# Performance work log

Hardware: AMD Instinct MI355X
Metric: run time of the kernel (lower is better)

Reference implementation:

```python
import jax, jax.numpy as jnp
import numpy as np

N_NODES = 100000
N_EDGES = 1600000
N_HOPS = 3
D_FEAT = 128
D_HID = 256
NUM_GRAPHS = 64


def setup_inputs() -> dict:
    key = jax.random.key(0)
    ks = jax.random.split(key, 8)
    x = jax.random.normal(ks[0], (N_NODES, D_FEAT), dtype=jnp.float32)
    edge_index = jax.random.randint(ks[1], (N_HOPS, 2, N_EDGES), 0, N_NODES, dtype=jnp.int64)
    edge_weight = jax.random.uniform(ks[2], (N_HOPS, N_EDGES), dtype=jnp.float32)
    batch = jnp.sort(jax.random.randint(ks[3], (N_NODES,), 0, NUM_GRAPHS, dtype=jnp.int64))
    w1 = jax.random.normal(ks[4], (D_FEAT, D_HID), dtype=jnp.float32) * (1.0 / np.sqrt(D_FEAT))
    b1 = jnp.zeros((D_HID,), dtype=jnp.float32)
    w2 = jax.random.normal(ks[5], (D_HID, D_FEAT), dtype=jnp.float32) * (1.0 / np.sqrt(D_HID))
    b2 = jnp.zeros((D_FEAT,), dtype=jnp.float32)
    prop_w = jnp.ones((N_HOPS + 1,), dtype=jnp.float32)
    return {"x": x, "edge_index": edge_index, "edge_weight": edge_weight,
            "batch": batch, "w1": w1, "b1": b1, "w2": w2, "b2": b2, "prop_w": prop_w}


def reference(x, edge_index, edge_weight, batch, w1, b1, w2, b2, prop_w):
    n = x.shape[0]
    # MLP: dropout is identity in eval mode
    h = jax.nn.relu(x @ w1 + b1)          # [N, hid]
    h = h @ w2 + b2                        # [N, feat]
    # prop_weight: weighted sum over hops; hop i uses edge_index[layers[i]-1]
    acc = prop_w[0] * h
    for i in range(edge_index.shape[0]):
        src = edge_index[i, 0]             # x_j source nodes
        dst = edge_index[i, 1]             # aggregation targets
        msg = edge_weight[i][:, None] * h[src]              # [E, feat]
        agg = jax.ops.segment_sum(msg, dst, num_segments=n)  # [N, feat]
        acc = acc + prop_w[i + 1] * agg
    # sum over hop dim already folded into acc; global_add_pool over graphs
    pooled = jax.ops.segment_sum(acc, batch, num_segments=NUM_GRAPHS)  # [G, feat]
    # original returns log_softmax of pooled features (lin3 output is unused)
    return jax.nn.log_softmax(pooled, axis=1)
```

## Files before the change

kernel.cpp:

```cpp
#include <hip/hip_runtime.h>
#include <hip/hip_bf16.h>


#define N_NODES 100000
#define N_EDGES 1600000
#define N_HOPS 3
#define D_HID 256
#define N_GRAPHS 64

#define CHUNK 32
#define NCHUNK 3125
#define FG 512

#define NB 625
#define RB 160
#define SGRID 500
#define SB 1024
#define I4PB 2400
#define NI4H 400000
#define STAGE_W 11475
#define RSTRIDE 11840

#define CT_OFF    0u
#define BU8_OFF   0u
#define REC_OFF   12800000u
#define SPART_OFF REC_OFF
#define OFFS_OFF  36500000u
#define SMALL_OFF 40000000u
#define TGR_OFF   SMALL_OFF
#define SSUM_OFF  (SMALL_OFF + 32768u)
#define W1P_OFF   (SMALL_OFF + 131072u)

typedef __attribute__((ext_vector_type(4))) float f32x4;
typedef __attribute__((ext_vector_type(8))) short s16x8;
typedef __attribute__((ext_vector_type(4))) int i32x4;
typedef __attribute__((ext_vector_type(4))) float fv4;

__device__ __forceinline__ unsigned short f2bf_rne(float f) {
    union { float f; unsigned u; } v; v.f = f;
    unsigned r = v.u + 0x7FFFu + ((v.u >> 16) & 1u);
    return (unsigned short)(r >> 16);
}
__device__ __forceinline__ float bf2f(unsigned short s) {
    union { float f; unsigned u; } v; v.u = ((unsigned)s) << 16;
    return v.f;
}
__device__ __forceinline__ unsigned pk_rne(float lo, float hi) {
    return ((unsigned)f2bf_rne(hi) << 16) | (unsigned)f2bf_rne(lo);
}

__global__ __launch_bounds__(256) void prep_kernel(const float* __restrict__ w1,
                                                   unsigned short* __restrict__ w1p,
                                                   const int* __restrict__ batch,
                                                   unsigned char* __restrict__ bu8) {
    if (blockIdx.x < 16) {
        int f = blockIdx.x * 256 + threadIdx.x;
        int t = f >> 4, fr = f & 15, nt = fr >> 2, ks = fr & 3;
        int w = t >> 6, l = t & 63, q = l >> 4, c = l & 15;
        s16x8 v;
#pragma unroll
        for (int j = 0; j < 8; j++)
            v[j] = (short)f2bf_rne(w1[(size_t)(32 * ks + 8 * q + j) * 256 + w * 64 + 16 * nt + c]);
        *(s16x8*)&w1p[(size_t)f * 8] = v;
    } else {
        int i = (blockIdx.x - 16) * 1024 + threadIdx.x * 4;
        if (i < N_NODES) {
            int4 v = *(const int4*)&batch[i];
            uchar4 o;
            o.x = (unsigned char)v.x; o.y = (unsigned char)v.y;
            o.z = (unsigned char)v.z; o.w = (unsigned char)v.w;
            *(uchar4*)&bu8[i] = o;
        }
    }
}

__global__ __launch_bounds__(SB) void scatter_kernel(
    const int* __restrict__ ei, const float* __restrict__ ew,
    const unsigned char* __restrict__ bu8, const float* __restrict__ pw,
    unsigned* __restrict__ offs, unsigned* __restrict__ records) {
    __shared__ unsigned cnt[NB], lbase[NB], ccnt[NB];
    __shared__ unsigned wtot[16];
    __shared__ unsigned tot;
    __shared__ unsigned stage[STAGE_W];
    const int tid = threadIdx.x;
    const int lane = tid & 63, wid = tid >> 6;
    const int i40 = blockIdx.x * I4PB;

    if (tid < NB) cnt[tid] = 0u;
    __syncthreads();

    const float pw1 = pw[1], pw2 = pw[2], pw3 = pw[3];

    unsigned rec[12], bkt[12];
#pragma unroll
    for (int k = 0; k < 3; k++) {
        int idx = tid + k * SB;
        if (idx < I4PB) {
            int i4 = i40 + idx;
            unsigned hop = (unsigned)i4 / NI4H;
            int r4 = i4 - (int)hop * NI4H;
            const i32x4* sp4 = (const i32x4*)(ei + (size_t)hop * 2 * N_EDGES);
            i32x4 s = __builtin_nontemporal_load(sp4 + r4);
            i32x4 d = __builtin_nontemporal_load(sp4 + NI4H + r4);
            fv4 wv = __builtin_nontemporal_load((const fv4*)(ew + (size_t)hop * N_EDGES) + r4);
            float pwh = hop == 0 ? pw1 : (hop == 1 ? pw2 : pw3);
#pragma unroll
            for (int j = 0; j < 4; j++) {
                unsigned b = (unsigned)s[j] / RB;
                bkt[k * 4 + j] = b;
                rec[k * 4 + j] = ((unsigned)f2bf_rne(pwh * wv[j]) << 16) |
                                 (unsigned)(((unsigned)s[j] - b * RB) * 64 + (unsigned)bu8[d[j]]);
                atomicAdd(&cnt[b], 1u);
            }
        } else {
#pragma unroll
            for (int j = 0; j < 4; j++) bkt[k * 4 + j] = 0xFFFFFFFFu;
        }
    }
    __syncthreads();

    unsigned pcv = 0;
    if (tid < NB) {
        unsigned cc = cnt[tid];
        ccnt[tid] = cc;
        pcv = (cc + 3u) & ~3u;
        cnt[tid] = 0u;
    }
    unsigned inc = pcv;
#pragma unroll
    for (int d = 1; d < 64; d <<= 1) {
        unsigned u = __shfl_up(inc, d, 64);
        if (lane >= d) inc += u;
    }
    if (lane == 63) wtot[wid] = inc;
    __syncthreads();
    if (tid < 16) {
        unsigned wv = wtot[tid];
        unsigned winc = wv;
#pragma unroll
        for (int d = 1; d < 16; d <<= 1) {
            unsigned u = __shfl_up(winc, d, 16);
            if ((tid & 15) >= d) winc += u;
        }
        wtot[tid] = winc - wv;
    }
    __syncthreads();
    if (tid < NB) {
        unsigned lb = inc - pcv + wtot[wid];
        lbase[tid] = lb;
        offs[(size_t)blockIdx.x * NB + tid] = (pcv << 16) | lb;
        if (tid == NB - 1) tot = lb + pcv;
        for (unsigned i = ccnt[tid]; i < pcv; i++) stage[lb + i] = 0u;
    }
    __syncthreads();

#pragma unroll
    for (int k = 0; k < 12; k++) {
        if (bkt[k] != 0xFFFFFFFFu) {
            unsigned o = atomicAdd(&cnt[bkt[k]], 1u);
            stage[lbase[bkt[k]] + o] = rec[k];
        }
    }
    __syncthreads();

    unsigned total = tot;
    unsigned* dst = records + (size_t)blockIdx.x * RSTRIDE;
    for (unsigned i = tid * 4; i < total; i += SB * 4) {
        *(uint4*)&dst[i] = *(const uint4*)&stage[i];
    }
}

__global__ __launch_bounds__(512) void phaseB_kernel(
    const int* __restrict__ batch, const float* __restrict__ pw,
    const unsigned* __restrict__ offs, const unsigned* __restrict__ records,
    unsigned short* __restrict__ ct, float* __restrict__ tgr) {
    __shared__ float tile[RB * 64];
    const int tid = threadIdx.x;
    const int b = blockIdx.x;
    const int grp = tid >> 3, gl = tid & 7;

    for (int i = tid; i < RB * 64; i += 512) tile[i] = 0.f;
    __syncthreads();

    if (tid < RB) atomicAdd(&tile[tid * 64 + batch[b * RB + tid]], pw[0]);

    for (int t = grp; t < SGRID; t += 64) {
        unsigned w = offs[(size_t)t * NB + b];
        const unsigned* rp = records + (size_t)t * RSTRIDE + (w & 0xFFFFu);
        unsigned pc = w >> 16;
        for (unsigned base = 4u * gl; base < pc; base += 32u) {
            uint4 r4 = *(const uint4*)(rp + base);
            unsigned m0 = r4.x & 0x3FFFu, m1 = r4.y & 0x3FFFu;
            unsigned m2 = r4.z & 0x3FFFu, m3 = r4.w & 0x3FFFu;
            atomicAdd(&tile[m0], bf2f((unsigned short)(r4.x >> 16)));
            atomicAdd(&tile[m1], bf2f((unsigned short)(r4.y >> 16)));
            atomicAdd(&tile[m2], bf2f((unsigned short)(r4.z >> 16)));
            atomicAdd(&tile[m3], bf2f((unsigned short)(r4.w >> 16)));
        }
    }
    __syncthreads();

    if (tid < 256) {
        const int gt = tid >> 6, l = tid & 63, q = l >> 4, c = l & 15;
        for (int cc = 0; cc < 5; cc++) {
            s16x8 v;
#pragma unroll
            for (int j = 0; j < 8; j++)
                v[j] = (short)f2bf_rne(tile[(cc * 32 + 8 * q + j) * 64 + 16 * gt + c]);
            *(s16x8*)&ct[(((size_t)(b * 5 + cc) * 4 + gt) * 64 + l) * 8] = v;
        }
    }
    if (tid < 64) {
        float sum = 0.f;
        for (int s = 0; s < RB; s++) sum += tile[s * 64 + tid];
        atomicAdd(&tgr[(b & 63) * 64 + tid], sum);
    }
}

__global__ __launch_bounds__(256, 2) void fused_kernel(
    const float* __restrict__ x,
    const unsigned short* __restrict__ w1p,
    const float* __restrict__ b1,
    const unsigned short* __restrict__ ct,
    unsigned short* __restrict__ s_part) {

    __shared__ __align__(16) unsigned short Ut[256 * 40];
    __shared__ __align__(16) unsigned short x_lds[32 * 136];
    __shared__ __align__(16) unsigned short ct_lds[2048];

    const int tid = threadIdx.x;
    const int w = tid >> 6, l = tid & 63, q = l >> 4, c = l & 15;
    const int wcol = w * 64;
    const int sr = tid >> 3, sk = (tid & 7) * 16;

    s16x8 w1f[4][4];
    {
        const s16x8* wp = (const s16x8*)(w1p + (size_t)tid * 128);
#pragma unroll
        for (int nt = 0; nt < 4; nt++)
#pragma unroll
            for (int ks = 0; ks < 4; ks++)
                w1f[nt][ks] = wp[nt * 4 + ks];
    }

    float bias[4];
#pragma unroll
    for (int nt = 0; nt < 4; nt++) bias[nt] = b1[wcol + 16 * nt + c];

    f32x4 sacc[4][4];
#pragma unroll
    for (int gt = 0; gt < 4; gt++)
#pragma unroll
        for (int nt = 0; nt < 4; nt++) sacc[gt][nt] = (f32x4)0.f;

    uint4 xp0, xp1;
    s16x8 ctp;

#define PREF(CI)                                                              \
    {                                                                         \
        const float4* p = (const float4*)&x[(size_t)((CI) * 32 + sr) * 128 + sk]; \
        float4 v0 = p[0], v1 = p[1], v2 = p[2], v3 = p[3];                    \
        xp0.x = pk_rne(v0.x, v0.y); xp0.y = pk_rne(v0.z, v0.w);               \
        xp0.z = pk_rne(v1.x, v1.y); xp0.w = pk_rne(v1.z, v1.w);               \
        xp1.x = pk_rne(v2.x, v2.y); xp1.y = pk_rne(v2.z, v2.w);               \
        xp1.z = pk_rne(v3.x, v3.y); xp1.w = pk_rne(v3.z, v3.w);               \
        ctp = *(const s16x8*)&ct[(size_t)(CI) * 2048 + tid * 8];              \
    }

    int ci = blockIdx.x;
    if (ci < NCHUNK) PREF(ci);

    for (; ci < NCHUNK; ci += FG) {
        *(uint4*)&x_lds[sr * 136 + sk] = xp0;
        *(uint4*)&x_lds[sr * 136 + sk + 8] = xp1;
        *(s16x8*)&ct_lds[tid * 8] = ctp;
        __syncthreads();

        s16x8 af[2][4], ctf[4];
#pragma unroll
        for (int mt = 0; mt < 2; mt++)
#pragma unroll
            for (int ks = 0; ks < 4; ks++)
                af[mt][ks] = *(const s16x8*)&x_lds[(16 * mt + c) * 136 + 32 * ks + 8 * q];
#pragma unroll
        for (int gt = 0; gt < 4; gt++)
            ctf[gt] = *(const s16x8*)&ct_lds[(gt * 64 + l) * 8];
        __syncthreads();

        if (ci + FG < NCHUNK) PREF(ci + FG);

        f32x4 u[2][4];
#pragma unroll
        for (int mt = 0; mt < 2; mt++)
#pragma unroll
            for (int nt = 0; nt < 4; nt++) {
                f32x4 a; a[0] = a[1] = a[2] = a[3] = bias[nt];
                u[mt][nt] = a;
            }
#pragma unroll
        for (int ks = 0; ks < 4; ks++)
#pragma unroll
            for (int mt = 0; mt < 2; mt++)
#pragma unroll
                for (int nt = 0; nt < 4; nt++)
                    u[mt][nt] = __builtin_amdgcn_mfma_f32_16x16x32_bf16(
                        af[mt][ks], w1f[nt][ks], u[mt][nt], 0, 0, 0);

#pragma unroll
        for (int mt = 0; mt < 2; mt++)
#pragma unroll
            for (int nt = 0; nt < 4; nt++) {
                f32x4 v = u[mt][nt];
                uint2 d;
                d.x = pk_rne(fmaxf(v[0], 0.f), fmaxf(v[1], 0.f));
                d.y = pk_rne(fmaxf(v[2], 0.f), fmaxf(v[3], 0.f));
                *(uint2*)&Ut[(wcol + 16 * nt + c) * 40 + 16 * mt + 4 * q] = d;
            }

#pragma unroll
        for (int nt = 0; nt < 4; nt++) {
            s16x8 uf = *(const s16x8*)&Ut[(wcol + 16 * nt + c) * 40 + 8 * q];
#pragma unroll
            for (int gt = 0; gt < 4; gt++)
                sacc[gt][nt] = __builtin_amdgcn_mfma_f32_16x16x32_bf16(
                    ctf[gt], uf, sacc[gt][nt], 0, 0, 0);
        }
    }
#undef PREF

    unsigned short* my = s_part + (size_t)blockIdx.x * (64 * 256);
#pragma unroll
    for (int gt = 0; gt < 4; gt++)
#pragma unroll
        for (int nt = 0; nt < 4; nt++)
#pragma unroll
            for (int r = 0; r < 4; r++)
                my[(16 * gt + 4 * q + r) * 256 + wcol + 16 * nt + c] =
                    f2bf_rne(sacc[gt][nt][r]);
}

__global__ __launch_bounds__(256) void reduce_kernel(const unsigned short* __restrict__ s_part,
                                                     float* __restrict__ s_sum) {
    __shared__ float red[4][64];
    const int l = threadIdx.x & 63, p = threadIdx.x >> 6;
    const int e = blockIdx.x * 64 + l;
    float a0 = 0.f, a1 = 0.f, a2 = 0.f, a3 = 0.f;
    for (int b = p * (FG / 4); b < (p + 1) * (FG / 4); b += 4) {
        a0 += bf2f(s_part[(size_t)(b + 0) * 16384 + e]);
        a1 += bf2f(s_part[(size_t)(b + 1) * 16384 + e]);
        a2 += bf2f(s_part[(size_t)(b + 2) * 16384 + e]);
        a3 += bf2f(s_part[(size_t)(b + 3) * 16384 + e]);
    }
    red[p][l] = (a0 + a1) + (a2 + a3);
    __syncthreads();
    if (p == 0) s_sum[e] = (red[0][l] + red[1][l]) + (red[2][l] + red[3][l]);
}

__global__ void finalize_kernel(const float* __restrict__ s,
                                const float* __restrict__ tgr,
                                const float* __restrict__ w2,
                                const float* __restrict__ b2,
                                float* __restrict__ out) {
    __shared__ float red[128];
    __shared__ float tgs;
    const int g = blockIdx.x;
    const int f = threadIdx.x;

    if (f < 64) {
        float v = tgr[f * 64 + g];
        for (int off = 32; off; off >>= 1) v += __shfl_down(v, off, 64);
        if (f == 0) tgs = v;
    }
    __syncthreads();

    float acc = tgs * b2[f];
    for (int k = 0; k < D_HID; k++)
        acc += s[(size_t)g * 256 + k] * w2[(size_t)k * 128 + f];

    red[f] = acc;
    __syncthreads();
    for (int off = 64; off > 0; off >>= 1) {
        if (f < off) red[f] = fmaxf(red[f], red[f + off]);
        __syncthreads();
    }
    float mx = red[0];
    __syncthreads();
    red[f] = expf(acc - mx);
    __syncthreads();
    for (int off = 64; off > 0; off >>= 1) {
        if (f < off) red[f] += red[f + off];
        __syncthreads();
    }
    float lse = logf(red[0]);
    out[(size_t)g * 128 + f] = acc - mx - lse;
}

extern "C" void kernel_launch(void* const* d_in, const int* in_sizes, int n_in,
                              void* d_out, int out_size, void* d_ws, size_t ws_size,
                              hipStream_t stream) {
    const float* x     = (const float*)d_in[0];
    const int*   ei    = (const int*)d_in[1];
    const float* ew    = (const float*)d_in[2];
    const int*   batch = (const int*)d_in[3];
    const float* w1    = (const float*)d_in[4];
    const float* b1    = (const float*)d_in[5];
    const float* w2    = (const float*)d_in[6];
    const float* b2    = (const float*)d_in[7];
    const float* pw    = (const float*)d_in[8];
    float* out = (float*)d_out;

    unsigned short* ctp     = (unsigned short*)((char*)d_ws + CT_OFF);
    unsigned char*  bu8     = (unsigned char*)((char*)d_ws + BU8_OFF);
    unsigned*       records = (unsigned*)((char*)d_ws + REC_OFF);
    unsigned short* s_part  = (unsigned short*)((char*)d_ws + SPART_OFF);
    unsigned*       offsp   = (unsigned*)((char*)d_ws + OFFS_OFF);
    float*          tgrp    = (float*)((char*)d_ws + TGR_OFF);
    float*          s_sum   = (float*)((char*)d_ws + SSUM_OFF);
    unsigned short* w1pp    = (unsigned short*)((char*)d_ws + W1P_OFF);

    hipMemsetAsync(tgrp, 0, 64 * 64 * sizeof(float), stream);

    prep_kernel<<<dim3(114), 256, 0, stream>>>(w1, w1pp, batch, bu8);
    scatter_kernel<<<dim3(SGRID), SB, 0, stream>>>(
        ei, ew, bu8, pw, offsp, records);
    phaseB_kernel<<<dim3(NB), 512, 0, stream>>>(batch, pw, offsp, records, ctp, tgrp);
    fused_kernel<<<dim3(FG), 256, 0, stream>>>(x, w1pp, b1, ctp, s_part);
    reduce_kernel<<<dim3(256), 256, 0, stream>>>(s_part, s_sum);
    finalize_kernel<<<dim3(64), 128, 0, stream>>>(s_sum, tgrp, w2, b2, out);
}
```

Measured before the change: 228.8 us.

## Replace two-pass bucketed scatter with direct global float atomics into coefficient matrix

The block-level bucket sort of edges into staged records, followed by a shared-memory accumulation pass, is replaced by a single kernel that does global float atomicAdd straight into a zeroed 100000x64 coefficient matrix C. A convert kernel then loads C tiles, adds the self term and emits the bf16 tiles. The aim is to drop the record write and read-back and the sorting overhead. In exchange it adds a 25.6MB memset and 4.8M scattered global atomics, which can contend. It also makes the accumulation order nondeterministic.

```diff
diff --git a/kernel.cpp b/kernel.cpp
--- a/kernel.cpp
+++ b/kernel.cpp
@@ -14,18 +14,15 @@
 
 #define NB 625
 #define RB 160
-#define SGRID 500
-#define SB 1024
-#define I4PB 2400
+#define NI4G 1200000
 #define NI4H 400000
-#define STAGE_W 11475
-#define RSTRIDE 11840
+#define AGG_BLOCKS 2048
+#define AGG_THREADS (AGG_BLOCKS * 256)
 
 #define CT_OFF    0u
-#define BU8_OFF   0u
-#define REC_OFF   12800000u
-#define SPART_OFF REC_OFF
-#define OFFS_OFF  36500000u
+#define C_OFF     12800000u
+#define SPART_OFF C_OFF
+#define BU8_OFF   38400000u
 #define SMALL_OFF 40000000u
 #define TGR_OFF   SMALL_OFF
 #define SSUM_OFF  (SMALL_OFF + 32768u)
@@ -74,130 +71,42 @@
     }
 }
 
-__global__ __launch_bounds__(SB) void scatter_kernel(
+__global__ __launch_bounds__(256) void agg_kernel(
     const int* __restrict__ ei, const float* __restrict__ ew,
     const unsigned char* __restrict__ bu8, const float* __restrict__ pw,
-    unsigned* __restrict__ offs, unsigned* __restrict__ records) {
-    __shared__ unsigned cnt[NB], lbase[NB], ccnt[NB];
-    __shared__ unsigned wtot[16];
-    __shared__ unsigned tot;
-    __shared__ unsigned stage[STAGE_W];
-    const int tid = threadIdx.x;
-    const int lane = tid & 63, wid = tid >> 6;
-    const int i40 = blockIdx.x * I4PB;
-
-    if (tid < NB) cnt[tid] = 0u;
-    __syncthreads();
-
+    float* __restrict__ C) {
     const float pw1 = pw[1], pw2 = pw[2], pw3 = pw[3];
-
-    unsigned rec[12], bkt[12];
-#pragma unroll
-    for (int k = 0; k < 3; k++) {
-        int idx = tid + k * SB;
-        if (idx < I4PB) {
-            int i4 = i40 + idx;
-            unsigned hop = (unsigned)i4 / NI4H;
-            int r4 = i4 - (int)hop * NI4H;
-            const i32x4* sp4 = (const i32x4*)(ei + (size_t)hop * 2 * N_EDGES);
-            i32x4 s = __builtin_nontemporal_load(sp4 + r4);
-            i32x4 d = __builtin_nontemporal_load(sp4 + NI4H + r4);
-            fv4 wv = __builtin_nontemporal_load((const fv4*)(ew + (size_t)hop * N_EDGES) + r4);
-            float pwh = hop == 0 ? pw1 : (hop == 1 ? pw2 : pw3);
-#pragma unroll
-            for (int j = 0; j < 4; j++) {
-                unsigned b = (unsigned)s[j] / RB;
-                bkt[k * 4 + j] = b;
-                rec[k * 4 + j] = ((unsigned)f2bf_rne(pwh * wv[j]) << 16) |
-                                 (unsigned)(((unsigned)s[j] - b * RB) * 64 + (unsigned)bu8[d[j]]);
-                atomicAdd(&cnt[b], 1u);
-            }
-        } else {
-#pragma unroll
-            for (int j = 0; j < 4; j++) bkt[k * 4 + j] = 0xFFFFFFFFu;
+    int gid = blockIdx.x * 256 + threadIdx.x;
+    for (int i4 = gid; i4 < NI4G; i4 += AGG_THREADS) {
+        unsigned hop = (unsigned)i4 / NI4H;
+        int r4 = i4 - (int)hop * NI4H;
+        const i32x4* sp4 = (const i32x4*)(ei + (size_t)hop * 2 * N_EDGES);
+        i32x4 s = __builtin_nontemporal_load(sp4 + r4);
+        i32x4 d = __builtin_nontemporal_load(sp4 + NI4H + r4);
+        fv4 wv = __builtin_nontemporal_load((const fv4*)(ew + (size_t)hop * N_EDGES) + r4);
+        float pwh = hop == 0 ? pw1 : (hop == 1 ? pw2 : pw3);
+#pragma unroll
+        for (int j = 0; j < 4; j++) {
+            unsigned g = bu8[d[j]];
+            atomicAdd(&C[(size_t)(unsigned)s[j] * 64 + g], pwh * wv[j]);
         }
     }
-    __syncthreads();
-
-    unsigned pcv = 0;
-    if (tid < NB) {
-        unsigned cc = cnt[tid];
-        ccnt[tid] = cc;
-        pcv = (cc + 3u) & ~3u;
-        cnt[tid] = 0u;
-    }
-    unsigned inc = pcv;
-#pragma unroll
-    for (int d = 1; d < 64; d <<= 1) {
-        unsigned u = __shfl_up(inc, d, 64);
-        if (lane >= d) inc += u;
-    }
-    if (lane == 63) wtot[wid] = inc;
-    __syncthreads();
-    if (tid < 16) {
-        unsigned wv = wtot[tid];
-        unsigned winc = wv;
-#pragma unroll
-        for (int d = 1; d < 16; d <<= 1) {
-            unsigned u = __shfl_up(winc, d, 16);
-            if ((tid & 15) >= d) winc += u;
-        }
-        wtot[tid] = winc - wv;
-    }
-    __syncthreads();
-    if (tid < NB) {
-        unsigned lb = inc - pcv + wtot[wid];
-        lbase[tid] = lb;
-        offs[(size_t)blockIdx.x * NB + tid] = (pcv << 16) | lb;
-        if (tid == NB - 1) tot = lb + pcv;
-        for (unsigned i = ccnt[tid]; i < pcv; i++) stage[lb + i] = 0u;
-    }
-    __syncthreads();
-
-#pragma unroll
-    for (int k = 0; k < 12; k++) {
-        if (bkt[k] != 0xFFFFFFFFu) {
-            unsigned o = atomicAdd(&cnt[bkt[k]], 1u);
-            stage[lbase[bkt[k]] + o] = rec[k];
-        }
-    }
-    __syncthreads();
-
-    unsigned total = tot;
-    unsigned* dst = records + (size_t)blockIdx.x * RSTRIDE;
-    for (unsigned i = tid * 4; i < total; i += SB * 4) {
-        *(uint4*)&dst[i] = *(const uint4*)&stage[i];
-    }
-}
-
-__global__ __launch_bounds__(512) void phaseB_kernel(
-    const int* __restrict__ batch, const float* __restrict__ pw,
-    const unsigned* __restrict__ offs, const unsigned* __restrict__ records,
+}
+
+__global__ __launch_bounds__(512) void convert_kernel(
+    const float* __restrict__ C, const unsigned char* __restrict__ bu8,
+    const float* __restrict__ pw,
     unsigned short* __restrict__ ct, float* __restrict__ tgr) {
     __shared__ float tile[RB * 64];
     const int tid = threadIdx.x;
     const int b = blockIdx.x;
-    const int grp = tid >> 3, gl = tid & 7;
-
-    for (int i = tid; i < RB * 64; i += 512) tile[i] = 0.f;
-    __syncthreads();
-
-    if (tid < RB) atomicAdd(&tile[tid * 64 + batch[b * RB + tid]], pw[0]);
-
-    for (int t = grp; t < SGRID; t += 64) {
-        unsigned w = offs[(size_t)t * NB + b];
-        const unsigned* rp = records + (size_t)t * RSTRIDE + (w & 0xFFFFu);
-        unsigned pc = w >> 16;
-        for (unsigned base = 4u * gl; base < pc; base += 32u) {
-            uint4 r4 = *(const uint4*)(rp + base);
-            unsigned m0 = r4.x & 0x3FFFu, m1 = r4.y & 0x3FFFu;
-            unsigned m2 = r4.z & 0x3FFFu, m3 = r4.w & 0x3FFFu;
-            atomicAdd(&tile[m0], bf2f((unsigned short)(r4.x >> 16)));
-            atomicAdd(&tile[m1], bf2f((unsigned short)(r4.y >> 16)));
-            atomicAdd(&tile[m2], bf2f((unsigned short)(r4.z >> 16)));
-            atomicAdd(&tile[m3], bf2f((unsigned short)(r4.w >> 16)));
-        }
-    }
+
+    const f32x4* src = (const f32x4*)(C + (size_t)b * RB * 64);
+    for (int i = tid; i < RB * 16; i += 512)
+        *(f32x4*)&tile[i * 4] = src[i];
+    __syncthreads();
+
+    if (tid < RB) tile[tid * 64 + bu8[b * RB + tid]] += pw[0];
     __syncthreads();
 
     if (tid < 256) {
@@ -410,20 +319,19 @@
     float* out = (float*)d_out;
 
     unsigned short* ctp     = (unsigned short*)((char*)d_ws + CT_OFF);
+    float*          Cp      = (float*)((char*)d_ws + C_OFF);
+    unsigned short* s_part  = (unsigned short*)((char*)d_ws + SPART_OFF);
     unsigned char*  bu8     = (unsigned char*)((char*)d_ws + BU8_OFF);
-    unsigned*       records = (unsigned*)((char*)d_ws + REC_OFF);
-    unsigned short* s_part  = (unsigned short*)((char*)d_ws + SPART_OFF);
-    unsigned*       offsp   = (unsigned*)((char*)d_ws + OFFS_OFF);
     float*          tgrp    = (float*)((char*)d_ws + TGR_OFF);
     float*          s_sum   = (float*)((char*)d_ws + SSUM_OFF);
     unsigned short* w1pp    = (unsigned short*)((char*)d_ws + W1P_OFF);
 
     hipMemsetAsync(tgrp, 0, 64 * 64 * sizeof(float), stream);
+    hipMemsetAsync(Cp, 0, (size_t)N_NODES * 64 * sizeof(float), stream);
 
     prep_kernel<<<dim3(114), 256, 0, stream>>>(w1, w1pp, batch, bu8);
-    scatter_kernel<<<dim3(SGRID), SB, 0, stream>>>(
-        ei, ew, bu8, pw, offsp, records);
-    phaseB_kernel<<<dim3(NB), 512, 0, stream>>>(batch, pw, offsp, records, ctp, tgrp);
+    agg_kernel<<<dim3(AGG_BLOCKS), 256, 0, stream>>>(ei, ew, bu8, pw, Cp);
+    convert_kernel<<<dim3(NB), 512, 0, stream>>>(Cp, bu8, pw, ctp, tgrp);
     fused_kernel<<<dim3(FG), 256, 0, stream>>>(x, w1pp, b1, ctp, s_part);
     reduce_kernel<<<dim3(256), 256, 0, stream>>>(s_part, s_sum);
     finalize_kernel<<<dim3(64), 128, 0, stream>>>(s_sum, tgrp, w2, b2, out);
```

Result: slower. 409.7 us (+79.1%).
